# Performance work log

Hardware: AMD Instinct MI355X
Metric: run time of the kernel (lower is better)

## Reference

```python
import jax, jax.numpy as jnp
import numpy as np

GRID_RES = 64
BOUND = 1.2

def _coords():
    lin = jnp.linspace(-BOUND, BOUND, GRID_RES, dtype=jnp.float32)
    gx, gy, gz = jnp.meshgrid(lin, lin, lin, indexing='ij')
    return jnp.stack([gx, gy, gz], axis=-1).reshape(-1, 3)  # (R^3, 3)

def setup_inputs() -> dict:
    key = jax.random.key(0)
    ks = jax.random.split(key, 9)
    B, D, H = 2, 512, 512
    s_in = 1.0 / np.sqrt(D + 3)
    s_h = 1.0 / np.sqrt(H)
    return {
        'cad_latent': jax.random.normal(ks[0], (B, D), jnp.float32),
        'W0': jax.random.normal(ks[1], (D + 3, H), jnp.float32) * s_in,
        'b0': jax.random.normal(ks[2], (H,), jnp.float32) * s_in,
        'W1': jax.random.normal(ks[3], (H, H), jnp.float32) * s_h,
        'b1': jax.random.normal(ks[4], (H,), jnp.float32) * s_h,
        'W2': jax.random.normal(ks[5], (H, H), jnp.float32) * s_h,
        'b2': jax.random.normal(ks[6], (H,), jnp.float32) * s_h,
        'W3': jax.random.normal(ks[7], (H, 1), jnp.float32) * s_h,
        'b3': jax.random.normal(ks[8], (1,), jnp.float32) * s_h,
    }

def reference(cad_latent, W0, b0, W1, b1, W2, b2, W3, b3):
    B, D = cad_latent.shape
    coords = _coords()  # (P, 3), P = R^3
    # First layer: concat([latent, coords]) @ W0 decomposed to avoid
    # materializing the broadcast-concatenated (B, P, D+3) tensor.
    lat_part = cad_latent @ W0[:D]          # (B, H)
    coord_part = coords @ W0[D:]            # (P, H)
    h = jax.nn.silu(lat_part[:, None, :] + coord_part[None, :, :] + b0)  # (B, P, H)
    h = jax.nn.silu(h @ W1 + b1)
    h = jax.nn.silu(h @ W2 + b2)
    sdf = h @ W3 + b3                       # (B, P, 1)
    return sdf.reshape(B, GRID_RES, GRID_RES, GRID_RES)
```

## Files before the change

kernel.cpp:

```cpp
#include <hip/hip_runtime.h>

#define H 512
#define MTILE 64
#define NBLK 8192
#define STEPC (2.4f / 63.0f)

typedef _Float16 half8 __attribute__((ext_vector_type(8)));
typedef _Float16 half4_t __attribute__((ext_vector_type(4)));
typedef float floatx16 __attribute__((ext_vector_type(16)));
typedef float floatx4 __attribute__((ext_vector_type(4)));
typedef float floatx2 __attribute__((ext_vector_type(2)));

__device__ inline float silu_f(float x) {
    return __fdividef(x, 1.0f + __expf(-x));
}

__global__ void prep_latw(const float* __restrict__ lat, const float* __restrict__ W0,
                          const float* __restrict__ b0, float* __restrict__ latw) {
    __shared__ float sl[H];
    const int b = blockIdx.x;
    const int j = threadIdx.x;
    sl[j] = lat[b * H + j];
    __syncthreads();
    float acc = b0[j];
#pragma unroll 8
    for (int d = 0; d < H; ++d) acc += sl[d] * W0[d * H + j];
    latw[b * H + j] = acc;
}

__global__ void prep_w16(const float* __restrict__ W1, const float* __restrict__ W2,
                         _Float16* __restrict__ ws) {
    const int id = blockIdx.x * 512 + threadIdx.x;
    const int l = id >> 18;
    const int rem = id & 0x3FFFF;
    const int k = rem >> 9, n = rem & 511;
    const float w = (l == 0 ? W1 : W2)[rem];
    ws[((size_t)(l * 64 + (k >> 3)) * 512 + n) * 8 + (k & 7)] = (_Float16)w;
}

__global__ __launch_bounds__(512, 4) void mesh_main(
    const float* __restrict__ W0, const float* __restrict__ b1,
    const float* __restrict__ b2, const float* __restrict__ W3,
    const float* __restrict__ b3, const float* __restrict__ latw,
    const _Float16* __restrict__ wsB, float* __restrict__ out) {

    __shared__ _Float16 hbuf2[4096 * 8];
    __shared__ float lwbuf[2 * H];
    __shared__ float partials[8][MTILE];

    const int tid = threadIdx.x;
    const int wave = tid >> 6, lane = tid & 63;
    const int lm = lane & 31, hi = lane >> 5;
    const int bi = blockIdx.x;
    const int b = bi >> 12;
    const int p0 = (bi & 4095) << 6;
    const float c0 = -1.2f + (float)(p0 >> 12) * STEPC;
    const float c1 = -1.2f + (float)((p0 >> 6) & 63) * STEPC;

    {
        const int j = tid;
        const float lwv = latw[b * H + j]
                        + c0 * W0[(H + 0) * H + j]
                        + c1 * W0[(H + 1) * H + j];
        floatx2 v;
        v[0] = lwv;
        v[1] = W0[(H + 2) * H + j];
        *(floatx2*)&lwbuf[2 * j] = v;
    }
    __syncthreads();

    {
        const float c2v = -1.2f + (float)lane * STEPC;
#pragma unroll
        for (int s = 0; s < 8; ++s) {
            const int g = wave * 8 + s;
            const floatx4* lp = (const floatx4*)&lwbuf[g * 16];
            half8 hv;
#pragma unroll
            for (int i = 0; i < 4; ++i) {
                const floatx4 pv = lp[i];
                hv[2 * i + 0] = (_Float16)silu_f(pv[0] + c2v * pv[1]);
                hv[2 * i + 1] = (_Float16)silu_f(pv[2] + c2v * pv[3]);
            }
            *(half8*)&hbuf2[(g * 64 + lane) * 8] = hv;
        }
    }

    const _Float16* hb = hbuf2 + hi * 512 + lm * 8;
    const _Float16* wsl = wsB + ((size_t)hi * 512 + wave * 64 + lm) * 8;

    floatx16 acc[2][2];

    auto zero_acc = [&]() {
#pragma unroll
        for (int mb = 0; mb < 2; ++mb)
#pragma unroll
            for (int nt = 0; nt < 2; ++nt)
#pragma unroll
                for (int r = 0; r < 16; ++r) acc[mb][nt][r] = 0.f;
    };

    auto loadW = [&](int l, int ks, half8 (&wf)[2]) {
        const _Float16* p = wsl + (size_t)(l * 32 + ks) * 8192;
        wf[0] = *(const half8*)(p);
        wf[1] = *(const half8*)(p + 256);
    };

    auto compute = [&](int ks, half8 (&wf)[2]) {
        half8 a[2];
        const _Float16* hp = hb + ks * 1024;
        a[0] = *(const half8*)(hp);
        a[1] = *(const half8*)(hp + 256);
#pragma unroll
        for (int nt = 0; nt < 2; ++nt)
#pragma unroll
            for (int mb = 0; mb < 2; ++mb)
                acc[mb][nt] = __builtin_amdgcn_mfma_f32_32x32x16_f16(wf[nt], a[mb], acc[mb][nt], 0, 0, 0);
    };

    auto run_gemm = [&](int l) {
        half8 Wb0[2], Wb1[2], Wb2[2], Wb3[2];
        loadW(l, 0, Wb0);
        loadW(l, 1, Wb1);
#pragma unroll 1
        for (int ks = 0; ks < 32; ks += 4) {
            loadW(l, (ks + 2) & 31, Wb2);
            compute(ks, Wb0);
            loadW(l, (ks + 3) & 31, Wb3);
            compute(ks + 1, Wb1);
            loadW(l, (ks + 4) & 31, Wb0);
            compute(ks + 2, Wb2);
            loadW(l, (ks + 5) & 31, Wb1);
            compute(ks + 3, Wb3);
        }
    };

    zero_acc();
    __syncthreads();
    run_gemm(0);
    __syncthreads();
    {
        _Float16* wb = hbuf2 + (wave * 8) * 512 + lm * 8 + hi * 4;
        floatx4 b1v[2][4];
#pragma unroll
        for (int nt = 0; nt < 2; ++nt)
#pragma unroll
            for (int g = 0; g < 4; ++g)
                b1v[nt][g] = *(const floatx4*)&b1[wave * 64 + nt * 32 + g * 8 + hi * 4];
#pragma unroll
        for (int mb = 0; mb < 2; ++mb)
#pragma unroll
            for (int nt = 0; nt < 2; ++nt)
#pragma unroll
                for (int g = 0; g < 4; ++g) {
                    half4_t hv;
#pragma unroll
                    for (int j = 0; j < 4; ++j)
                        hv[j] = (_Float16)silu_f(acc[mb][nt][g * 4 + j] + b1v[nt][g][j]);
                    *(half4_t*)(wb + (nt * 4 + g) * 512 + mb * 256) = hv;
                }
    }

    zero_acc();
    __syncthreads();
    run_gemm(1);

    {
        floatx4 b2v[2][4], w3v[2][4];
#pragma unroll
        for (int nt = 0; nt < 2; ++nt)
#pragma unroll
            for (int g = 0; g < 4; ++g) {
                const int n0 = wave * 64 + nt * 32 + g * 8 + hi * 4;
                b2v[nt][g] = *(const floatx4*)&b2[n0];
                w3v[nt][g] = *(const floatx4*)&W3[n0];
            }
#pragma unroll
        for (int mb = 0; mb < 2; ++mb) {
            float sum = 0.f;
#pragma unroll
            for (int nt = 0; nt < 2; ++nt)
#pragma unroll
                for (int g = 0; g < 4; ++g)
#pragma unroll
                    for (int j = 0; j < 4; ++j)
                        sum += silu_f(acc[mb][nt][g * 4 + j] + b2v[nt][g][j]) * w3v[nt][g][j];
            sum += __shfl_xor(sum, 32);
            if (hi == 0) partials[wave][mb * 32 + lm] = sum;
        }
    }
    __syncthreads();
    if (tid < MTILE) {
        float o = b3[0];
#pragma unroll
        for (int w = 0; w < 8; ++w) o += partials[w][tid];
        out[(size_t)bi * MTILE + tid] = o;
    }
}

extern "C" void kernel_launch(void* const* d_in, const int* in_sizes, int n_in,
                              void* d_out, int out_size, void* d_ws, size_t ws_size,
                              hipStream_t stream) {
    const float* lat = (const float*)d_in[0];
    const float* W0  = (const float*)d_in[1];
    const float* b0  = (const float*)d_in[2];
    const float* W1  = (const float*)d_in[3];
    const float* b1  = (const float*)d_in[4];
    const float* W2  = (const float*)d_in[5];
    const float* b2  = (const float*)d_in[6];
    const float* W3  = (const float*)d_in[7];
    const float* b3  = (const float*)d_in[8];
    float* out = (float*)d_out;

    float* latw = (float*)d_ws;
    _Float16* wsB = (_Float16*)((char*)d_ws + 4096);

    prep_latw<<<2, 512, 0, stream>>>(lat, W0, b0, latw);
    prep_w16<<<1024, 512, 0, stream>>>(W1, W2, wsB);
    mesh_main<<<NBLK, 512, 0, stream>>>(W0, b1, b2, W3, b3, latw, wsB, out);
}
```

Before: 835.8 us.

## Fuse prep kernels, reorder weight layout per wave, deepen GEMM prefetch pipeline

```diff
diff --git a/kernel.cpp b/kernel.cpp
--- a/kernel.cpp
+++ b/kernel.cpp
@@ -15,30 +15,34 @@
     return __fdividef(x, 1.0f + __expf(-x));
 }
 
-__global__ void prep_latw(const float* __restrict__ lat, const float* __restrict__ W0,
-                          const float* __restrict__ b0, float* __restrict__ latw) {
+__global__ void prep_fused(const float* __restrict__ lat, const float* __restrict__ W0,
+                           const float* __restrict__ b0,
+                           const float* __restrict__ W1, const float* __restrict__ W2,
+                           float* __restrict__ latw, _Float16* __restrict__ ws) {
     __shared__ float sl[H];
-    const int b = blockIdx.x;
-    const int j = threadIdx.x;
-    sl[j] = lat[b * H + j];
-    __syncthreads();
-    float acc = b0[j];
+    if (blockIdx.x < 1024) {
+        const int id = blockIdx.x * 512 + threadIdx.x;
+        const int l = id >> 18;
+        const int rem = id & 0x3FFFF;
+        const int k = rem >> 9, n = rem & 511;
+        const float w = (l == 0 ? W1 : W2)[rem];
+        const int ks = k >> 4, hi = (k >> 3) & 1, e = k & 7;
+        const int wv = n >> 6, nt = (n >> 5) & 1, lm = n & 31;
+        ws[(size_t)(l * 8 + wv) * 32768 + hi * 16384 + ks * 512 + nt * 256 + lm * 8 + e]
+            = (_Float16)w;
+    } else {
+        const int b = blockIdx.x - 1024;
+        const int j = threadIdx.x;
+        sl[j] = lat[b * H + j];
+        __syncthreads();
+        float acc = b0[j];
 #pragma unroll 8
-    for (int d = 0; d < H; ++d) acc += sl[d] * W0[d * H + j];
-    latw[b * H + j] = acc;
-}
-
-__global__ void prep_w16(const float* __restrict__ W1, const float* __restrict__ W2,
-                         _Float16* __restrict__ ws) {
-    const int id = blockIdx.x * 512 + threadIdx.x;
-    const int l = id >> 18;
-    const int rem = id & 0x3FFFF;
-    const int k = rem >> 9, n = rem & 511;
-    const float w = (l == 0 ? W1 : W2)[rem];
-    ws[((size_t)(l * 64 + (k >> 3)) * 512 + n) * 8 + (k & 7)] = (_Float16)w;
-}
-
-__global__ __launch_bounds__(512, 4) void mesh_main(
+        for (int d = 0; d < H; ++d) acc += sl[d] * W0[d * H + j];
+        latw[b * H + j] = acc;
+    }
+}
+
+__global__ __launch_bounds__(512, 2) void mesh_main(
     const float* __restrict__ W0, const float* __restrict__ b1,
     const float* __restrict__ b2, const float* __restrict__ W3,
     const float* __restrict__ b3, const float* __restrict__ latw,
@@ -51,6 +55,7 @@
     const int tid = threadIdx.x;
     const int wave = tid >> 6, lane = tid & 63;
     const int lm = lane & 31, hi = lane >> 5;
+    const int uwave = __builtin_amdgcn_readfirstlane(wave);
     const int bi = blockIdx.x;
     const int b = bi >> 12;
     const int p0 = (bi & 4095) << 6;
@@ -87,7 +92,7 @@
     }
 
     const _Float16* hb = hbuf2 + hi * 512 + lm * 8;
-    const _Float16* wsl = wsB + ((size_t)hi * 512 + wave * 64 + lm) * 8;
+    const int vWoff = hi * 16384 + lm * 8;
 
     floatx16 acc[2][2];
 
@@ -100,17 +105,19 @@
                 for (int r = 0; r < 16; ++r) acc[mb][nt][r] = 0.f;
     };
 
-    auto loadW = [&](int l, int ks, half8 (&wf)[2]) {
-        const _Float16* p = wsl + (size_t)(l * 32 + ks) * 8192;
+    auto loadW = [&](const _Float16* base, int ks, half8 (&wf)[2]) {
+        const _Float16* p = base + vWoff + ks * 512;
         wf[0] = *(const half8*)(p);
         wf[1] = *(const half8*)(p + 256);
     };
 
-    auto compute = [&](int ks, half8 (&wf)[2]) {
-        half8 a[2];
+    auto loadA = [&](int ks, half8 (&a)[2]) {
         const _Float16* hp = hb + ks * 1024;
         a[0] = *(const half8*)(hp);
         a[1] = *(const half8*)(hp + 256);
+    };
+
+    auto compute = [&](half8 (&wf)[2], half8 (&a)[2]) {
 #pragma unroll
         for (int nt = 0; nt < 2; ++nt)
 #pragma unroll
@@ -118,26 +125,27 @@
                 acc[mb][nt] = __builtin_amdgcn_mfma_f32_32x32x16_f16(wf[nt], a[mb], acc[mb][nt], 0, 0, 0);
     };
 
-    auto run_gemm = [&](int l) {
-        half8 Wb0[2], Wb1[2], Wb2[2], Wb3[2];
-        loadW(l, 0, Wb0);
-        loadW(l, 1, Wb1);
-#pragma unroll 1
-        for (int ks = 0; ks < 32; ks += 4) {
-            loadW(l, (ks + 2) & 31, Wb2);
-            compute(ks, Wb0);
-            loadW(l, (ks + 3) & 31, Wb3);
-            compute(ks + 1, Wb1);
-            loadW(l, (ks + 4) & 31, Wb0);
-            compute(ks + 2, Wb2);
-            loadW(l, (ks + 5) & 31, Wb1);
-            compute(ks + 3, Wb3);
+    auto run_gemm = [&](const _Float16* base) {
+        half8 Wq[6][2];
+        half8 Aq[3][2];
+#pragma unroll
+        for (int i = 0; i < 6; ++i) loadW(base, i, Wq[i]);
+#pragma unroll
+        for (int i = 0; i < 3; ++i) loadA(i, Aq[i]);
+#pragma unroll
+        for (int ks = 0; ks < 32; ++ks) {
+            compute(Wq[ks % 6], Aq[ks % 3]);
+            if (ks + 6 < 32) loadW(base, ks + 6, Wq[ks % 6]);
+            if (ks + 3 < 32) loadA(ks + 3, Aq[ks % 3]);
         }
     };
 
+    const _Float16* wbase0 = wsB + (size_t)uwave * 32768;
+    const _Float16* wbase1 = wsB + (size_t)(8 + uwave) * 32768;
+
     zero_acc();
     __syncthreads();
-    run_gemm(0);
+    run_gemm(wbase0);
     __syncthreads();
     {
         _Float16* wb = hbuf2 + (wave * 8) * 512 + lm * 8 + hi * 4;
@@ -163,7 +171,7 @@
 
     zero_acc();
     __syncthreads();
-    run_gemm(1);
+    run_gemm(wbase1);
 
     {
         floatx4 b2v[2][4], w3v[2][4];
@@ -215,7 +223,6 @@
     float* latw = (float*)d_ws;
     _Float16* wsB = (_Float16*)((char*)d_ws + 4096);
 
-    prep_latw<<<2, 512, 0, stream>>>(lat, W0, b0, latw);
-    prep_w16<<<1024, 512, 0, stream>>>(W1, W2, wsB);
+    prep_fused<<<1026, 512, 0, stream>>>(lat, W0, b0, W1, W2, latw, wsB);
     mesh_main<<<NBLK, 512, 0, stream>>>(W0, b1, b2, W3, b3, latw, wsB, out);
 }
```

New measurement: 810.9 us. 1.03x faster.
